# Kernel tuning notes

Measured on AMD Instinct MI355X. Metric: run time of the kernel, lower is better.

Reference implementation:

```python
import jax, jax.numpy as jnp
import numpy as np

B, N, F, DM, DMO, OM, L = 32, 64, 64, 128, 64, 128, 4
PRE_H, PRE_O, POST_H = 128, 64, 64
E = N * N
EPS = 1e-5


def swish(x):
    return x * jax.nn.sigmoid(x)


def bn_edges(x, g, b):
    # BatchNorm1d(num_features=E) applied to [B, E, D]: per-edge-channel stats over (batch, D)
    m = x.mean(axis=(0, 2), keepdims=True)
    v = x.var(axis=(0, 2), keepdims=True)
    return (x - m) / jnp.sqrt(v + EPS) * g[None, :, None] + b[None, :, None]


def setup_inputs():
    key = jax.random.key(0)
    ks = iter(jax.random.split(key, 64))

    def rn(shape, s=0.05):
        return jax.random.normal(next(ks), shape, dtype=jnp.float32) * s

    # fully-connected graph incl. self-loops (required by BatchNorm1d(n_nodes^2))
    src, dst = np.meshgrid(np.arange(N), np.arange(N), indexing='ij')
    edge_index = jnp.asarray(np.stack([src.reshape(-1), dst.reshape(-1)]), dtype=jnp.int32)
    return {
        'node_feature': rn((B, N, F), 1.0),
        'vectors': rn((B, N, OM), 1.0),
        'edge_index': edge_index,
        'msg_W1': rn((L, 2 * F, DM)), 'msg_b1': rn((L, DM)),
        'bn1_g': jnp.ones((L, E), jnp.float32), 'bn1_b': jnp.zeros((L, E), jnp.float32),
        'msg_W2': rn((L, DM, DM)), 'msg_b2': rn((L, DM)),
        'bn2_g': jnp.ones((L, E), jnp.float32), 'bn2_b': jnp.zeros((L, E), jnp.float32),
        'msg_W3': rn((L, DM, DM)), 'msg_b3': rn((L, DM)),
        'bn3_g': jnp.ones((L, E), jnp.float32), 'bn3_b': jnp.zeros((L, E), jnp.float32),
        'msg_W4': rn((L, DM, DMO)), 'msg_b4': rn((L, DMO)),
        'upd_W1': rn((L, OM + F + DMO, DM)), 'upd_b1': rn((L, DM)),
        'upd_W2': rn((L, DM, DM)), 'upd_b2': rn((L, DM)),
        'upd_W3': rn((L, DM, DM)), 'upd_b3': rn((L, DM)),
        'upd_W4': rn((L, DM, F)), 'upd_b4': rn((L, F)),
        'pre_W1': rn((F, PRE_H)), 'pre_b1': rn((PRE_H,)),
        'pre_W2': rn((PRE_H, PRE_H)), 'pre_b2': rn((PRE_H,)),
        'pre_W3': rn((PRE_H, PRE_H)), 'pre_b3': rn((PRE_H,)),
        'pre_W4': rn((PRE_H, PRE_O)), 'pre_b4': rn((PRE_O,)),
        'post_W1': rn((PRE_O, POST_H)), 'post_b1': rn((POST_H,)),
        'post_W2': rn((POST_H, 1)), 'post_b2': rn((1,)),
    }


def reference(node_feature, vectors, edge_index,
              msg_W1, msg_b1, bn1_g, bn1_b, msg_W2, msg_b2, bn2_g, bn2_b,
              msg_W3, msg_b3, bn3_g, bn3_b, msg_W4, msg_b4,
              upd_W1, upd_b1, upd_W2, upd_b2, upd_W3, upd_b3, upd_W4, upd_b4,
              pre_W1, pre_b1, pre_W2, pre_b2, pre_W3, pre_b3, pre_W4, pre_b4,
              post_W1, post_b1, post_W2, post_b2):
    src, dst = edge_index[0], edge_index[1]
    x = node_feature  # [B, N, F]
    v = vectors       # [B, N, OM]
    cnt = jax.ops.segment_sum(jnp.ones((E,), jnp.float32), dst, num_segments=N)
    inv_cnt = 1.0 / jnp.maximum(cnt, 1.0)
    for l in range(L):
        x_i = x[:, dst]  # [B, E, F] gather targets
        x_j = x[:, src]  # [B, E, F] gather sources
        h = swish(jnp.concatenate([x_i, x_j], -1) @ msg_W1[l] + msg_b1[l])
        h = bn_edges(h, bn1_g[l], bn1_b[l])
        h = bn_edges(swish(h @ msg_W2[l] + msg_b2[l]), bn2_g[l], bn2_b[l])
        h = bn_edges(swish(h @ msg_W3[l] + msg_b3[l]), bn3_g[l], bn3_b[l])
        m = swish(h @ msg_W4[l] + msg_b4[l])  # [B, E, DMO]
        agg = jax.ops.segment_sum(jnp.transpose(m, (1, 0, 2)), dst, num_segments=N)
        agg = jnp.transpose(agg, (1, 0, 2)) * inv_cnt[None, :, None]  # mean aggr, [B, N, DMO]
        u = jnp.concatenate([v, x, agg], -1)  # [B, N, OM+F+DMO]
        h = swish(u @ upd_W1[l] + upd_b1[l])
        h = swish(h @ upd_W2[l] + upd_b2[l])
        h = swish(h @ upd_W3[l] + upd_b3[l])
        x = x + swish(h @ upd_W4[l] + upd_b4[l])  # residual update
    h = swish(x @ pre_W1 + pre_b1)
    h = swish(h @ pre_W2 + pre_b2)
    h = swish(h @ pre_W3 + pre_b3)
    h = h @ pre_W4 + pre_b4
    c = swish(h @ post_W1 + post_b1) @ post_W2 + post_b2  # [B, N, 1]
    x3 = jnp.einsum('bnd,bn->bd', v, c[..., 0])           # coefficient-weighted vector sum
    return x3, v, c
```

## Files before the change

### kernel.cpp

```cpp
#include <hip/hip_runtime.h>
#include <hip/hip_bf16.h>

typedef unsigned short u16t;
typedef __attribute__((ext_vector_type(8))) short bf16x8;
typedef __attribute__((ext_vector_type(4))) short bf16x4;
typedef __attribute__((ext_vector_type(4))) float f32x4;

#define Bn 32
#define Nn 64
#define Fd 64
#define DMd 128
#define DMOd 64
#define OMd 128
#define En 4096

#define NTEN 36
#define TOTALC 1073217
#define HP 136
#define UP 264
#define XP 72
#define WSEG 131072

__device__ const int kOffs[NTEN + 1] = {
    0,        131072,   393216,   458752,   459264,   475648,   492032,   557568,
    558080,   574464,   590848,   656384,   656896,   673280,   689664,   722432,
    722688,   853760,   854272,   919808,   920320,   985856,   986368,   1019136,
    1019392,  1027584,  1027712,  1044096,  1044224,  1060608,  1060736,  1068928,
    1068992,  1073088,  1073152,  1073216,  1073217
};

#define C_NF    0
#define C_VEC   131072
#define C_MW1   393216
#define C_MB1   458752
#define C_G1    459264
#define C_BB1   475648
#define C_MW2   492032
#define C_MB2   557568
#define C_G2    558080
#define C_BB2   574464
#define C_MW3   590848
#define C_MB3   656384
#define C_G3    656896
#define C_BB3   673280
#define C_MW4   689664
#define C_MB4   722432
#define C_UW1   722688
#define C_UB1   853760
#define C_UW2   854272
#define C_UB2   919808
#define C_UW3   920320
#define C_UB3   985856
#define C_UW4   986368
#define C_UB4   1019136
#define C_PW1   1019392
#define C_PB1   1027584
#define C_PW2   1027712
#define C_PB2   1044096
#define C_PW3   1044224
#define C_PB3   1060608
#define C_PW4   1060736
#define C_PB4   1068928
#define C_QW1   1068992
#define C_QB1   1073088
#define C_QW2   1073152
#define C_QB2   1073216

#define S_W2T 0
#define S_W3T 16384
#define S_W4T 32768
#define S_U1T 40960
#define S_U2T 73728
#define S_U3T 90112
#define S_U4T 106496
#define S_W1T 114688

__device__ const int liveStart[9] = {0, C_MB1, C_MB2, C_MB3, C_MB4, C_UB1, C_UB2, C_UB3, C_UB4};
__device__ const int livePre[10]  = {0, 393216, 426496, 459776, 493056, 493312, 493824, 494336, 494848, 548929};
#define NCOMPACT 548929

#define NB_CONV 2145
#define NB_PREPW 2048
#define NB_CS 5
#define NB_PQ0 1024
#define NB_PREP (NB_CONV + NB_PREPW + NB_CS + NB_PQ0)

struct Ptrs { const void* p[NTEN]; };

__device__ __forceinline__ float us2f(u16t u) {
    return __uint_as_float(((unsigned int)u) << 16);
}
__device__ __forceinline__ u16t f2us(float f) {
    __hip_bfloat16 h = __float2bfloat16(f);
    return *reinterpret_cast<u16t*>(&h);
}
__device__ __forceinline__ float swishf(float x) {
    return x * __builtin_amdgcn_rcpf(1.0f + __expf(-x));
}
__device__ __forceinline__ float ldcvt(const void* p, int idx, int flag) {
    return flag ? us2f(((const u16t*)p)[idx]) : ((const float*)p)[idx];
}
__device__ __forceinline__ int get_flag(const void* g1raw) {
    return (((const u16t*)g1raw)[0] == 0x3F80u) ? 1 : 0;
}

__global__ __launch_bounds__(256) void k_prep(Ptrs t, float* __restrict__ C,
                                              float* __restrict__ x,
                                              u16t* __restrict__ W,
                                              float* __restrict__ CS,
                                              float* __restrict__ P,
                                              float* __restrict__ Q,
                                              float* __restrict__ agg) {
    const int flag = get_flag(t.p[4]);
    const int blk = blockIdx.x;
    const int tid = threadIdx.x;

    if (blk < NB_CONV) {
        int i = blk * 256 + tid;
        if (i >= NCOMPACT) return;
        int lo = 0, hi = 9;
        while (hi - lo > 1) { int m = (lo + hi) >> 1; if (i >= livePre[m]) lo = m; else hi = m; }
        const int Cidx = liveStart[lo] + (i - livePre[lo]);
        int lo2 = 0, hi2 = NTEN;
        while (hi2 - lo2 > 1) { int m = (lo2 + hi2) >> 1; if (Cidx >= kOffs[m]) lo2 = m; else hi2 = m; }
        float v = ldcvt(t.p[lo2], Cidx - kOffs[lo2], flag);
        if (Cidx < Bn * Nn * Fd) x[Cidx] = v;
        else                     C[Cidx] = v;
    } else if (blk < NB_CONV + NB_PREPW) {
        int i = (blk - NB_CONV) * 256 + tid;
        const int l = i / WSEG;
        int r = i - l * WSEG;
        int tens, local;
        if (r < S_W3T)      { int q = r;          int n = q >> 7, k = q & 127; tens = 6;  local = l*16384 + k*128 + n; }
        else if (r < S_W4T) { int q = r - S_W3T;  int n = q >> 7, k = q & 127; tens = 10; local = l*16384 + k*128 + n; }
        else if (r < S_U1T) { int q = r - S_W4T;  int n = q >> 7, k = q & 127; tens = 14; local = l*8192  + k*64  + n; }
        else if (r < S_U2T) { int q = r - S_U1T;  int n = q >> 8, k = q & 255; tens = 16; local = l*32768 + k*128 + n; }
        else if (r < S_U3T) { int q = r - S_U2T;  int n = q >> 7, k = q & 127; tens = 18; local = l*16384 + k*128 + n; }
        else if (r < S_U4T) { int q = r - S_U3T;  int n = q >> 7, k = q & 127; tens = 20; local = l*16384 + k*128 + n; }
        else if (r < S_W1T) { int q = r - S_U4T;  int n = q >> 7, k = q & 127; tens = 22; local = l*8192  + k*64  + n; }
        else                { int q = r - S_W1T;  int n = q >> 7, k = q & 127; tens = 2;  local = l*16384 + k*128 + n; }
        W[i] = f2us(ldcvt(t.p[tens], local, flag));
    } else if (blk < NB_CONV + NB_PREPW + NB_CS) {
        int i = (blk - NB_CONV - NB_PREPW) * 256 + tid;
        if (i >= 4 * 320) return;
        const int l = i / 320, j = i - l * 320;
        const void* tp; int base, stride;
        if (j < 128)      { tp = t.p[6];  base = l*16384 + j;         stride = 128; }
        else if (j < 256) { tp = t.p[10]; base = l*16384 + (j - 128); stride = 128; }
        else              { tp = t.p[14]; base = l*8192  + (j - 256); stride = 64; }
        float s = 0.f;
        #pragma unroll 8
        for (int k = 0; k < 128; k++) s += us2f(f2us(ldcvt(tp, base + k * stride, flag)));
        CS[i] = s;
    } else {
        const int rel = blk - (NB_CONV + NB_PREPW + NB_CS);
        const int gid = rel * 256 + tid;
        if (gid < Bn * Nn * DMOd) agg[gid] = 0.f;
        __shared__ float xr2[2][Fd];
        const int half = tid >> 7, t7 = tid & 127;
        const int bn = rel * 2 + half;
        if (t7 < Fd) xr2[half][t7] = ldcvt(t.p[0], bn * Fd + t7, flag);
        __syncthreads();
        float accP = 0.f, accQ = 0.f;
        if (flag) {
            const u16t* W1 = (const u16t*)t.p[2];
            #pragma unroll 8
            for (int k = 0; k < Fd; k++) {
                float xv = xr2[half][k];
                accP += xv * us2f(W1[k * DMd + t7]);
                accQ += xv * us2f(W1[(Fd + k) * DMd + t7]);
            }
        } else {
            const float* W1 = (const float*)t.p[2];
            #pragma unroll 8
            for (int k = 0; k < Fd; k++) {
                float xv = xr2[half][k];
                accP += xv * W1[k * DMd + t7];
                accQ += xv * W1[(Fd + k) * DMd + t7];
            }
        }
        P[bn * DMd + t7] = accP + ldcvt(t.p[3], t7, flag);
        Q[bn * DMd + t7] = accQ;
    }
}

__device__ __forceinline__ void wave_red8(float* s, float (*rd)[8], int wv, int lane) {
    #pragma unroll
    for (int off = 32; off > 0; off >>= 1)
        #pragma unroll
        for (int k = 0; k < 8; k++) s[k] += __shfl_down(s[k], off);
    if (lane == 0) {
        #pragma unroll
        for (int k = 0; k < 8; k++) rd[wv][k] = s[k];
    }
}

__device__ __forceinline__ void calc_ab(const float (*rd)[8],
                                        const float* __restrict__ g,
                                        const float* __restrict__ bb,
                                        int src0, int dst,
                                        float* a, float* c) {
    #pragma unroll
    for (int e = 0; e < 4; e++) {
        float S  = rd[0][2*e]   + rd[1][2*e]   + rd[2][2*e]   + rd[3][2*e];
        float S2 = rd[0][2*e+1] + rd[1][2*e+1] + rd[2][2*e+1] + rd[3][2*e+1];
        float mean = S * (1.0f / 4096.0f);
        float var  = S2 * (1.0f / 4096.0f) - mean * mean;
        float av = rsqrtf(var + 1e-5f) * g[(src0 + e) * Nn + dst];
        a[e] = av;
        c[e] = bb[(src0 + e) * Nn + dst] - mean * av;
    }
}

__global__ __launch_bounds__(256, 4) void k_edge(
    const float* __restrict__ P, const float* __restrict__ Q,
    const float* __restrict__ g1, const float* __restrict__ bb1,
    const u16t* __restrict__ W2t, const float* __restrict__ b2v, const float* __restrict__ cs2,
    const float* __restrict__ g2, const float* __restrict__ bb2,
    const u16t* __restrict__ W3t, const float* __restrict__ b3v, const float* __restrict__ cs3,
    const float* __restrict__ g3, const float* __restrict__ bb3,
    const u16t* __restrict__ W4t, const float* __restrict__ b4v, const float* __restrict__ cs4,
    float* __restrict__ agg) {
    __shared__ u16t hE[4][Bn * HP];
    __shared__ float red[2][4][8];

    const int dst = blockIdx.x & 63, src0 = (blockIdx.x >> 6) * 4;
    const int tid = threadIdx.x;
    const int wv = tid >> 6, lane = tid & 63, quad = lane >> 4, l15 = lane & 15;
    const int mw = wv & 1, nb2 = wv >> 1;
    const int mrow = mw * 16 + l15;
    const int nBase = nb2 * 64;

    {
        const int b = tid >> 3, d0 = (tid & 7) * 16;
        float4 pv[4];
        {
            const float4* pp = (const float4*)&P[(b * Nn + dst) * DMd + d0];
            #pragma unroll
            for (int j = 0; j < 4; j++) pv[j] = pp[j];
        }
        float s[8];
        #pragma unroll
        for (int e = 0; e < 4; e++) {
            const float4* qq = (const float4*)&Q[(b * Nn + src0 + e) * DMd + d0];
            float u[16];
            #pragma unroll
            for (int j = 0; j < 4; j++) {
                float4 qv = qq[j];
                u[j*4+0] = swishf(pv[j].x + qv.x);
                u[j*4+1] = swishf(pv[j].y + qv.y);
                u[j*4+2] = swishf(pv[j].z + qv.z);
                u[j*4+3] = swishf(pv[j].w + qv.w);
            }
            float se = 0.f, s2e = 0.f;
            #pragma unroll
            for (int i = 0; i < 16; i++) { se += u[i]; s2e += u[i] * u[i]; }
            bf16x8 s0, s1;
            #pragma unroll
            for (int j = 0; j < 8; j++) {
                s0[j] = (short)f2us(u[j]);
                s1[j] = (short)f2us(u[8 + j]);
            }
            *(bf16x8*)&hE[e][b * HP + d0]     = s0;
            *(bf16x8*)&hE[e][b * HP + d0 + 8] = s1;
            s[2*e] = se; s[2*e+1] = s2e;
        }
        wave_red8(s, red[0], wv, lane);
    }
    __syncthreads();

    float aP[4], cP[4];
    calc_ab(red[0], g1, bb1, src0, dst, aP, cP);

    #pragma unroll 1
    for (int st = 0; st < 2; st++) {
        const u16t*  Wt = st ? W3t : W2t;
        const float* bv = st ? b3v : b2v;
        const float* cv = st ? cs3 : cs2;
        f32x4 acc[4][4];
        #pragma unroll
        for (int e = 0; e < 4; e++)
            #pragma unroll
            for (int t = 0; t < 4; t++) acc[e][t] = (f32x4){0.f, 0.f, 0.f, 0.f};
        #pragma unroll
        for (int ks = 0; ks < 4; ks++) {
            bf16x8 wb[4];
            #pragma unroll
            for (int t = 0; t < 4; t++)
                wb[t] = *(const bf16x8*)&Wt[(nBase + t * 16 + l15) * 128 + ks * 32 + quad * 8];
            #pragma unroll
            for (int e = 0; e < 4; e++) {
                bf16x8 a8 = *(const bf16x8*)&hE[e][mrow * HP + ks * 32 + quad * 8];
                #pragma unroll
                for (int t = 0; t < 4; t++)
                    acc[e][t] = __builtin_amdgcn_mfma_f32_16x16x32_bf16(wb[t], a8, acc[e][t], 0, 0, 0);
            }
        }
        bf16x4 pk[4][4];
        float s[8];
        #pragma unroll
        for (int e = 0; e < 4; e++) {
            const float ae = aP[e], ce = cP[e];
            float se = 0.f, s2e = 0.f;
            #pragma unroll
            for (int t = 0; t < 4; t++) {
                const int n0 = nBase + t * 16 + quad * 4;
                float4 c4  = *(const float4*)&cv[n0];
                float4 bb4 = *(const float4*)&bv[n0];
                #pragma unroll
                for (int r = 0; r < 4; r++) {
                    float z = ae * acc[e][t][r] + (ce * (&c4.x)[r] + (&bb4.x)[r]);
                    float u = swishf(z);
                    se += u; s2e += u * u;
                    pk[e][t][r] = (short)f2us(u);
                }
            }
            s[2*e] = se; s[2*e+1] = s2e;
        }
        wave_red8(s, red[1 - st], wv, lane);
        __syncthreads();
        calc_ab(red[1 - st], st ? g3 : g2, st ? bb3 : bb2, src0, dst, aP, cP);
        #pragma unroll
        for (int e = 0; e < 4; e++)
            #pragma unroll
            for (int t = 0; t < 4; t++)
                *(bf16x4*)&hE[e][mrow * HP + nBase + t * 16 + quad * 4] = pk[e][t];
        __syncthreads();
    }

    {
        const int n40 = nb2 * 32;
        f32x4 a4[4][2];
        #pragma unroll
        for (int e = 0; e < 4; e++) {
            a4[e][0] = (f32x4){0.f, 0.f, 0.f, 0.f};
            a4[e][1] = (f32x4){0.f, 0.f, 0.f, 0.f};
        }
        #pragma unroll
        for (int ks = 0; ks < 4; ks++) {
            bf16x8 wb[2];
            #pragma unroll
            for (int t = 0; t < 2; t++)
                wb[t] = *(const bf16x8*)&W4t[(n40 + t * 16 + l15) * 128 + ks * 32 + quad * 8];
            #pragma unroll
            for (int e = 0; e < 4; e++) {
                bf16x8 a8 = *(const bf16x8*)&hE[e][mrow * HP + ks * 32 + quad * 8];
                #pragma unroll
                for (int t = 0; t < 2; t++)
                    a4[e][t] = __builtin_amdgcn_mfma_f32_16x16x32_bf16(a8, wb[t], a4[e][t], 0, 0, 0);
            }
        }
        #pragma unroll
        for (int t = 0; t < 2; t++) {
            const int col = n40 + t * 16 + l15;
            const float csv = cs4[col], bvv = b4v[col];
            float fe[4];
            #pragma unroll
            for (int e = 0; e < 4; e++) fe[e] = cP[e] * csv + bvv;
            #pragma unroll
            for (int r = 0; r < 4; r++) {
                float m = swishf(aP[0] * a4[0][t][r] + fe[0])
                        + swishf(aP[1] * a4[1][t][r] + fe[1])
                        + swishf(aP[2] * a4[2][t][r] + fe[2])
                        + swishf(aP[3] * a4[3][t][r] + fe[3]);
                const int b = mw * 16 + quad * 4 + r;
                atomicAdd(&agg[(b * Nn + dst) * DMOd + col], m);
            }
        }
    }
}

__global__ __launch_bounds__(256, 4) void k_updq(
    const float* __restrict__ vC, float* __restrict__ x, float* __restrict__ agg,
    const u16t* __restrict__ U1t, const float* __restrict__ b1,
    const u16t* __restrict__ U2t, const float* __restrict__ b2,
    const u16t* __restrict__ U3t, const float* __restrict__ b3,
    const u16t* __restrict__ U4t, const float* __restrict__ b4,
    const u16t* __restrict__ W1Tn, const float* __restrict__ b1n,
    float* __restrict__ Pn, float* __restrict__ Qn,
    int doPQ) {
    __shared__ u16t uL[16 * UP];
    __shared__ u16t hL[16 * HP];
    __shared__ u16t xL[16 * XP];
    const int g0 = blockIdx.x * 16;
    const int tid = threadIdx.x;
    const int wv = tid >> 6, lane = tid & 63, quad = lane >> 4, l15 = lane & 15;
    const int nBase = wv * 32;

    {
        const int i = tid >> 4, c0 = (tid & 15) * 16;
        const int g = g0 + i;
        const float* srcp; float scl = 1.f;
        if (c0 < 128)       srcp = &vC[g * OMd + c0];
        else if (c0 < 192)  srcp = &x[g * Fd + (c0 - 128)];
        else              { srcp = &agg[g * DMOd + (c0 - 192)]; scl = 1.0f / 64.0f; }
        bf16x8 s0, s1;
        #pragma unroll
        for (int j = 0; j < 8; j++) {
            s0[j] = (short)f2us(srcp[j] * scl);
            s1[j] = (short)f2us(srcp[8 + j] * scl);
        }
        *(bf16x8*)&uL[i * UP + c0]     = s0;
        *(bf16x8*)&uL[i * UP + c0 + 8] = s1;
    }
    __syncthreads();

    {
        f32x4 acc[2];
        #pragma unroll
        for (int t = 0; t < 2; t++) {
            float b0 = b1[nBase + t * 16 + l15];
            acc[t] = (f32x4){b0, b0, b0, b0};
        }
        #pragma unroll
        for (int ks = 0; ks < 8; ks++) {
            bf16x8 a8 = *(const bf16x8*)&uL[l15 * UP + ks * 32 + quad * 8];
            #pragma unroll
            for (int t = 0; t < 2; t++) {
                bf16x8 b8 = *(const bf16x8*)&U1t[(nBase + t * 16 + l15) * 256 + ks * 32 + quad * 8];
                acc[t] = __builtin_amdgcn_mfma_f32_16x16x32_bf16(a8, b8, acc[t], 0, 0, 0);
            }
        }
        #pragma unroll
        for (int t = 0; t < 2; t++)
            #pragma unroll
            for (int r = 0; r < 4; r++)
                hL[(quad * 4 + r) * HP + nBase + t * 16 + l15] = f2us(swishf(acc[t][r]));
    }
    __syncthreads();

    #pragma unroll 1
    for (int st = 0; st < 2; st++) {
        const u16t*  Ut = st ? U3t : U2t;
        const float* bb = st ? b3  : b2;
        f32x4 acc[2];
        #pragma unroll
        for (int t = 0; t < 2; t++) {
            float b0 = bb[nBase + t * 16 + l15];
            acc[t] = (f32x4){b0, b0, b0, b0};
        }
        #pragma unroll
        for (int ks = 0; ks < 4; ks++) {
            bf16x8 a8 = *(const bf16x8*)&hL[l15 * HP + ks * 32 + quad * 8];
            #pragma unroll
            for (int t = 0; t < 2; t++) {
                bf16x8 b8 = *(const bf16x8*)&Ut[(nBase + t * 16 + l15) * 128 + ks * 32 + quad * 8];
                acc[t] = __builtin_amdgcn_mfma_f32_16x16x32_bf16(a8, b8, acc[t], 0, 0, 0);
            }
        }
        __syncthreads();
        #pragma unroll
        for (int t = 0; t < 2; t++)
            #pragma unroll
            for (int r = 0; r < 4; r++)
                hL[(quad * 4 + r) * HP + nBase + t * 16 + l15] = f2us(swishf(acc[t][r]));
        __syncthreads();
    }

    {
        const int n4 = wv * 16;
        f32x4 acc;
        {
            float b0 = b4[n4 + l15];
            acc = (f32x4){b0, b0, b0, b0};
        }
        #pragma unroll
        for (int ks = 0; ks < 4; ks++) {
            bf16x8 a8 = *(const bf16x8*)&hL[l15 * HP + ks * 32 + quad * 8];
            bf16x8 b8 = *(const bf16x8*)&U4t[(n4 + l15) * 128 + ks * 32 + quad * 8];
            acc = __builtin_amdgcn_mfma_f32_16x16x32_bf16(a8, b8, acc, 0, 0, 0);
        }
        #pragma unroll
        for (int r = 0; r < 4; r++) {
            int row = quad * 4 + r, col = n4 + l15;
            float xn = x[(g0 + row) * Fd + col] + swishf(acc[r]);
            x[(g0 + row) * Fd + col] = xn;
            xL[row * XP + col] = f2us(xn);
        }
    }

    {
        int idx = tid;
        #pragma unroll
        for (int k = 0; k < 4; k++, idx += 256) agg[g0 * DMOd + idx] = 0.f;
    }
    __syncthreads();

    if (doPQ) {
        f32x4 ap[2], aq[2];
        #pragma unroll
        for (int j = 0; j < 2; j++) { ap[j] = (f32x4){0,0,0,0}; aq[j] = (f32x4){0,0,0,0}; }
        #pragma unroll
        for (int ks = 0; ks < 2; ks++) {
            bf16x8 a8 = *(const bf16x8*)&xL[l15 * XP + ks * 32 + quad * 8];
            #pragma unroll
            for (int j = 0; j < 2; j++) {
                const int n0 = (wv * 2 + j) * 16 + l15;
                bf16x8 bp = *(const bf16x8*)&W1Tn[n0 * 128 + ks * 32 + quad * 8];
                bf16x8 bq = *(const bf16x8*)&W1Tn[n0 * 128 + 64 + ks * 32 + quad * 8];
                ap[j] = __builtin_amdgcn_mfma_f32_16x16x32_bf16(a8, bp, ap[j], 0, 0, 0);
                aq[j] = __builtin_amdgcn_mfma_f32_16x16x32_bf16(a8, bq, aq[j], 0, 0, 0);
            }
        }
        #pragma unroll
        for (int j = 0; j < 2; j++)
            #pragma unroll
            for (int r = 0; r < 4; r++) {
                int g = g0 + quad * 4 + r, col = (wv * 2 + j) * 16 + l15;
                Pn[g * DMd + col] = ap[j][r] + b1n[col];
                Qn[g * DMd + col] = aq[j][r];
            }
    }
}

__global__ __launch_bounds__(128) void k_final(
    const float* __restrict__ x, const void* __restrict__ vraw,
    const float* __restrict__ pW1, const float* __restrict__ pb1,
    const float* __restrict__ pW2, const float* __restrict__ pb2,
    const float* __restrict__ pW3, const float* __restrict__ pb3,
    const float* __restrict__ pW4, const float* __restrict__ pb4,
    const float* __restrict__ qW1, const float* __restrict__ qb1,
    const float* __restrict__ qW2, const float* __restrict__ qb2,
    float* __restrict__ c_buf, void* __restrict__ out, const void* __restrict__ g1raw) {
    __shared__ float xr[64];
    __shared__ float ha[128];
    __shared__ float hb[128];
    __shared__ float hc[64];
    __shared__ float tt[64];
    const int bn = blockIdx.x;
    const int tid = threadIdx.x;
    const int flag = get_flag(g1raw);
    if (tid < 64) xr[tid] = x[bn * Fd + tid];
    __syncthreads();
    float acc = pb1[tid];
    #pragma unroll 8
    for (int k = 0; k < 64; k++) acc += xr[k] * pW1[k * 128 + tid];
    ha[tid] = swishf(acc);
    __syncthreads();
    acc = pb2[tid];
    #pragma unroll 8
    for (int k = 0; k < 128; k++) acc += ha[k] * pW2[k * 128 + tid];
    hb[tid] = swishf(acc);
    __syncthreads();
    acc = pb3[tid];
    #pragma unroll 8
    for (int k = 0; k < 128; k++) acc += hb[k] * pW3[k * 128 + tid];
    ha[tid] = swishf(acc);
    __syncthreads();
    if (tid < 64) {
        acc = pb4[tid];
        #pragma unroll 8
        for (int k = 0; k < 128; k++) acc += ha[k] * pW4[k * 64 + tid];
        hc[tid] = acc;
    }
    __syncthreads();
    if (tid < 64) {
        acc = qb1[tid];
        #pragma unroll 8
        for (int k = 0; k < 64; k++) acc += hc[k] * qW1[k * 64 + tid];
        tt[tid] = swishf(acc);
    }
    __syncthreads();
    if (tid < 64) {
        float p = tt[tid] * qW2[tid];
        #pragma unroll
        for (int off = 32; off > 0; off >>= 1) p += __shfl_down(p, off);
        if (tid == 0) {
            float cv = p + qb2[0];
            c_buf[bn] = cv;
            const int ci = 4096 + Bn * Nn * OMd + bn;
            if (flag) ((u16t*)out)[ci] = f2us(cv);
            else      ((float*)out)[ci] = cv;
        }
    }
    const int vi = bn * OMd + tid;
    if (flag) ((u16t*)out)[4096 + vi] = ((const u16t*)vraw)[vi];
    else      ((float*)out)[4096 + vi] = ((const float*)vraw)[vi];
}

__global__ __launch_bounds__(128) void k_x3(const float* __restrict__ vC,
                                            const float* __restrict__ c_buf,
                                            void* __restrict__ out,
                                            const void* __restrict__ g1raw) {
    const int b = blockIdx.x, d = threadIdx.x;
    const int flag = get_flag(g1raw);
    float acc = 0.f;
    #pragma unroll 4
    for (int n = 0; n < Nn; n++)
        acc += vC[(b * Nn + n) * OMd + d] * c_buf[b * Nn + n];
    if (flag) ((u16t*)out)[b * OMd + d] = f2us(acc);
    else      ((float*)out)[b * OMd + d] = acc;
}

extern "C" void kernel_launch(void* const* d_in, const int* in_sizes, int n_in,
                              void* d_out, int out_size, void* d_ws, size_t ws_size,
                              hipStream_t stream) {
    float* ws = (float*)d_ws;
    float* C     = ws + 16;
    float* x     = C + 1073664;
    float* P     = x + 131072;
    float* Q     = P + 262144;
    float* agg   = Q + 262144;
    float* c_buf = agg + 131072;
    u16t*  Wt    = (u16t*)(c_buf + 2048);
    float* CS    = (float*)(Wt + 4 * WSEG);

    Ptrs t;
    for (int i = 0, j = 0; i < 37; i++) {
        if (i == 2) continue;
        t.p[j++] = d_in[i];
    }

    k_prep<<<NB_PREP, 256, 0, stream>>>(t, C, x, Wt, CS, P, Q, agg);

    for (int l = 0; l < 4; l++) {
        u16t* Wl = Wt + l * WSEG;
        float* CSl = CS + l * 320;
        k_edge<<<64 * 16, 256, 0, stream>>>(
            P, Q,
            C + C_G1 + l * En, C + C_BB1 + l * En,
            Wl + S_W2T, C + C_MB2 + l * DMd, CSl,
            C + C_G2 + l * En, C + C_BB2 + l * En,
            Wl + S_W3T, C + C_MB3 + l * DMd, CSl + 128,
            C + C_G3 + l * En, C + C_BB3 + l * En,
            Wl + S_W4T, C + C_MB4 + l * DMOd, CSl + 256,
            agg);
        const int doPQ = (l < 3) ? 1 : 0;
        const u16t* W1Tn = Wt + (doPQ ? (l + 1) : 0) * WSEG + S_W1T;
        const float* b1n = C + C_MB1 + (doPQ ? (l + 1) : 0) * DMd;
        k_updq<<<Bn * Nn / 16, 256, 0, stream>>>(
            C + C_VEC, x, agg,
            Wl + S_U1T, C + C_UB1 + l * DMd,
            Wl + S_U2T, C + C_UB2 + l * DMd,
            Wl + S_U3T, C + C_UB3 + l * DMd,
            Wl + S_U4T, C + C_UB4 + l * DMOd,
            W1Tn, b1n, P, Q, doPQ);
    }

    k_final<<<Bn * Nn, 128, 0, stream>>>(x, d_in[1],
        C + C_PW1, C + C_PB1, C + C_PW2, C + C_PB2,
        C + C_PW3, C + C_PB3, C + C_PW4, C + C_PB4,
        C + C_QW1, C + C_QB1, C + C_QW2, C + C_QB2,
        c_buf, d_out, d_in[5]);
    k_x3<<<Bn, 128, 0, stream>>>(C + C_VEC, c_buf, d_out, d_in[5]);
}
```

Measured before the change: 360.9 us.

## Fuse final MLP head into last update kernel and move vectors copy into prep

The separate k_final launch is removed. The last-layer k_updq now keeps the updated node features in fp32 shared memory and runs the pre/post MLP head itself, two nodes at a time across 8 iterations per block. The passthrough copy of the vectors output moves into extra blocks of k_prep. This saves one kernel launch and the round trip of x through global memory, but only 128 blocks do the head sequentially with many barriers, which cuts parallelism for that stage.

```diff
diff --git a/kernel.cpp b/kernel.cpp
--- a/kernel.cpp
+++ b/kernel.cpp
@@ -83,7 +83,8 @@
 #define NB_PREPW 2048
 #define NB_CS 5
 #define NB_PQ0 1024
-#define NB_PREP (NB_CONV + NB_PREPW + NB_CS + NB_PQ0)
+#define NB_VC 256
+#define NB_PREP (NB_CONV + NB_PREPW + NB_CS + NB_PQ0 + NB_VC)
 
 struct Ptrs { const void* p[NTEN]; };
 
@@ -110,7 +111,8 @@
                                               float* __restrict__ CS,
                                               float* __restrict__ P,
                                               float* __restrict__ Q,
-                                              float* __restrict__ agg) {
+                                              float* __restrict__ agg,
+                                              void* __restrict__ out) {
     const int flag = get_flag(t.p[4]);
     const int blk = blockIdx.x;
     const int tid = threadIdx.x;
@@ -152,7 +154,7 @@
         #pragma unroll 8
         for (int k = 0; k < 128; k++) s += us2f(f2us(ldcvt(tp, base + k * stride, flag)));
         CS[i] = s;
-    } else {
+    } else if (blk < NB_CONV + NB_PREPW + NB_CS + NB_PQ0) {
         const int rel = blk - (NB_CONV + NB_PREPW + NB_CS);
         const int gid = rel * 256 + tid;
         if (gid < Bn * Nn * DMOd) agg[gid] = 0.f;
@@ -181,6 +183,25 @@
         }
         P[bn * DMd + t7] = accP + ldcvt(t.p[3], t7, flag);
         Q[bn * DMd + t7] = accQ;
+    } else {
+        const int base = (blk - (NB_CONV + NB_PREPW + NB_CS + NB_PQ0)) * 1024;
+        if (flag) {
+            const u16t* src = (const u16t*)t.p[1];
+            u16t* dst = (u16t*)out;
+            #pragma unroll
+            for (int j = 0; j < 4; j++) {
+                const int idx = base + j * 256 + tid;
+                dst[4096 + idx] = src[idx];
+            }
+        } else {
+            const float* src = (const float*)t.p[1];
+            float* dst = (float*)out;
+            #pragma unroll
+            for (int j = 0; j < 4; j++) {
+                const int idx = base + j * 256 + tid;
+                dst[4096 + idx] = src[idx];
+            }
+        }
     }
 }
 
@@ -378,10 +399,14 @@
     const u16t* __restrict__ U4t, const float* __restrict__ b4,
     const u16t* __restrict__ W1Tn, const float* __restrict__ b1n,
     float* __restrict__ Pn, float* __restrict__ Qn,
+    const float* __restrict__ Ch, float* __restrict__ c_buf,
+    void* __restrict__ out, const void* __restrict__ g1raw,
     int doPQ) {
     __shared__ u16t uL[16 * UP];
     __shared__ u16t hL[16 * HP];
     __shared__ u16t xL[16 * XP];
+    __shared__ float xF[16][68];
+    __shared__ float hsc[2][384];
     const int g0 = blockIdx.x * 16;
     const int tid = threadIdx.x;
     const int wv = tid >> 6, lane = tid & 63, quad = lane >> 4, l15 = lane & 15;
@@ -475,7 +500,8 @@
             int row = quad * 4 + r, col = n4 + l15;
             float xn = x[(g0 + row) * Fd + col] + swishf(acc[r]);
             x[(g0 + row) * Fd + col] = xn;
-            xL[row * XP + col] = f2us(xn);
+            if (doPQ) xL[row * XP + col] = f2us(xn);
+            else      xF[row][col] = xn;
         }
     }
 
@@ -510,72 +536,62 @@
                 Pn[g * DMd + col] = ap[j][r] + b1n[col];
                 Qn[g * DMd + col] = aq[j][r];
             }
-    }
-}
-
-__global__ __launch_bounds__(128) void k_final(
-    const float* __restrict__ x, const void* __restrict__ vraw,
-    const float* __restrict__ pW1, const float* __restrict__ pb1,
-    const float* __restrict__ pW2, const float* __restrict__ pb2,
-    const float* __restrict__ pW3, const float* __restrict__ pb3,
-    const float* __restrict__ pW4, const float* __restrict__ pb4,
-    const float* __restrict__ qW1, const float* __restrict__ qb1,
-    const float* __restrict__ qW2, const float* __restrict__ qb2,
-    float* __restrict__ c_buf, void* __restrict__ out, const void* __restrict__ g1raw) {
-    __shared__ float xr[64];
-    __shared__ float ha[128];
-    __shared__ float hb[128];
-    __shared__ float hc[64];
-    __shared__ float tt[64];
-    const int bn = blockIdx.x;
-    const int tid = threadIdx.x;
-    const int flag = get_flag(g1raw);
-    if (tid < 64) xr[tid] = x[bn * Fd + tid];
-    __syncthreads();
-    float acc = pb1[tid];
-    #pragma unroll 8
-    for (int k = 0; k < 64; k++) acc += xr[k] * pW1[k * 128 + tid];
-    ha[tid] = swishf(acc);
-    __syncthreads();
-    acc = pb2[tid];
-    #pragma unroll 8
-    for (int k = 0; k < 128; k++) acc += ha[k] * pW2[k * 128 + tid];
-    hb[tid] = swishf(acc);
-    __syncthreads();
-    acc = pb3[tid];
-    #pragma unroll 8
-    for (int k = 0; k < 128; k++) acc += hb[k] * pW3[k * 128 + tid];
-    ha[tid] = swishf(acc);
-    __syncthreads();
-    if (tid < 64) {
-        acc = pb4[tid];
-        #pragma unroll 8
-        for (int k = 0; k < 128; k++) acc += ha[k] * pW4[k * 64 + tid];
-        hc[tid] = acc;
-    }
-    __syncthreads();
-    if (tid < 64) {
-        acc = qb1[tid];
-        #pragma unroll 8
-        for (int k = 0; k < 64; k++) acc += hc[k] * qW1[k * 64 + tid];
-        tt[tid] = swishf(acc);
-    }
-    __syncthreads();
-    if (tid < 64) {
-        float p = tt[tid] * qW2[tid];
-        #pragma unroll
-        for (int off = 32; off > 0; off >>= 1) p += __shfl_down(p, off);
-        if (tid == 0) {
-            float cv = p + qb2[0];
-            c_buf[bn] = cv;
-            const int ci = 4096 + Bn * Nn * OMd + bn;
-            if (flag) ((u16t*)out)[ci] = f2us(cv);
-            else      ((float*)out)[ci] = cv;
-        }
-    }
-    const int vi = bn * OMd + tid;
-    if (flag) ((u16t*)out)[4096 + vi] = ((const u16t*)vraw)[vi];
-    else      ((float*)out)[4096 + vi] = ((const float*)vraw)[vi];
+    } else {
+        const int half = tid >> 7, t7 = tid & 127;
+        const float* pW1 = Ch + C_PW1; const float* pb1h = Ch + C_PB1;
+        const float* pW2 = Ch + C_PW2; const float* pb2h = Ch + C_PB2;
+        const float* pW3 = Ch + C_PW3; const float* pb3h = Ch + C_PB3;
+        const float* pW4 = Ch + C_PW4; const float* pb4h = Ch + C_PB4;
+        const float* qW1 = Ch + C_QW1; const float* qb1h = Ch + C_QB1;
+        const float* qW2 = Ch + C_QW2; const float* qb2h = Ch + C_QB2;
+        const int flag = get_flag(g1raw);
+        float* ha = &hsc[half][0];
+        float* hb = &hsc[half][128];
+        float* hc = &hsc[half][256];
+        #pragma unroll 1
+        for (int p = 0; p < 8; p++) {
+            const int node = p * 2 + half;
+            const int bn = g0 + node;
+            float acc = pb1h[t7];
+            #pragma unroll 8
+            for (int k = 0; k < 64; k++) acc += xF[node][k] * pW1[k * 128 + t7];
+            ha[t7] = swishf(acc);
+            __syncthreads();
+            acc = pb2h[t7];
+            #pragma unroll 8
+            for (int k = 0; k < 128; k++) acc += ha[k] * pW2[k * 128 + t7];
+            hb[t7] = swishf(acc);
+            __syncthreads();
+            acc = pb3h[t7];
+            #pragma unroll 8
+            for (int k = 0; k < 128; k++) acc += hb[k] * pW3[k * 128 + t7];
+            ha[t7] = swishf(acc);
+            __syncthreads();
+            if (t7 < 64) {
+                acc = pb4h[t7];
+                #pragma unroll 8
+                for (int k = 0; k < 128; k++) acc += ha[k] * pW4[k * 64 + t7];
+                hc[t7] = acc;
+            }
+            __syncthreads();
+            if (t7 < 64) {
+                acc = qb1h[t7];
+                #pragma unroll 8
+                for (int k = 0; k < 64; k++) acc += hc[k] * qW1[k * 64 + t7];
+                float pv = swishf(acc) * qW2[t7];
+                #pragma unroll
+                for (int off = 32; off > 0; off >>= 1) pv += __shfl_down(pv, off);
+                if (t7 == 0) {
+                    float cv = pv + qb2h[0];
+                    c_buf[bn] = cv;
+                    const int ci = 4096 + Bn * Nn * OMd + bn;
+                    if (flag) ((u16t*)out)[ci] = f2us(cv);
+                    else      ((float*)out)[ci] = cv;
+                }
+            }
+            __syncthreads();
+        }
+    }
 }
 
 __global__ __launch_bounds__(128) void k_x3(const float* __restrict__ vC,
@@ -611,7 +627,7 @@
         t.p[j++] = d_in[i];
     }
 
-    k_prep<<<NB_PREP, 256, 0, stream>>>(t, C, x, Wt, CS, P, Q, agg);
+    k_prep<<<NB_PREP, 256, 0, stream>>>(t, C, x, Wt, CS, P, Q, agg, d_out);
 
     for (int l = 0; l < 4; l++) {
         u16t* Wl = Wt + l * WSEG;
@@ -634,13 +650,9 @@
             Wl + S_U2T, C + C_UB2 + l * DMd,
             Wl + S_U3T, C + C_UB3 + l * DMd,
             Wl + S_U4T, C + C_UB4 + l * DMOd,
-            W1Tn, b1n, P, Q, doPQ);
-    }
-
-    k_final<<<Bn * Nn, 128, 0, stream>>>(x, d_in[1],
-        C + C_PW1, C + C_PB1, C + C_PW2, C + C_PB2,
-        C + C_PW3, C + C_PB3, C + C_PW4, C + C_PB4,
-        C + C_QW1, C + C_QB1, C + C_QW2, C + C_QB2,
-        c_buf, d_out, d_in[5]);
+            W1Tn, b1n, P, Q,
+            C, c_buf, d_out, d_in[5], doPQ);
+    }
+
     k_x3<<<Bn, 128, 0, stream>>>(C + C_VEC, c_buf, d_out, d_in[5]);
 }
```

Measured after the change: 443.8 us. 23.0% more time.
